# Kernel optimization log

Hardware: AMD Instinct MI355X
Metric: run time of the kernel (lower is better)

Reference implementation:

```python
import jax, jax.numpy as jnp
import numpy as np

B, L, C, H, W = 4, 16, 64, 64, 64
F, NH, NB = 128, 2, 2


def _ln(x, w, b, eps=1e-5):
    # LayerNorm over last two dims (H, W), torch-style biased variance
    m = jnp.mean(x, axis=(-2, -1), keepdims=True)
    v = jnp.var(x, axis=(-2, -1), keepdims=True)
    return (x - m) * jax.lax.rsqrt(v + eps) * w + b


def _conv2d(x, w, b):
    # x: (N, Cin, H, W), w: (Cout, Cin, k, k) -- the (1,k,k) Conv3d acts per-frame
    y = jax.lax.conv_general_dilated(x, w, (1, 1), 'SAME',
                                     dimension_numbers=('NCHW', 'OIHW', 'NCHW'))
    return y + b[None, :, None, None]


def _combine(c1, c2):
    a1, b1 = c1
    a2, b2 = c2
    return a1 * a2, a2 * b1 + b2


def _forward(x, params_log, pBw_r, pBw_i, pBb_r, pBb_i, pCw_r, pCw_i, pCb_r, pCb_i,
             lru_ln_w, lru_ln_b, cin_w, cin_b, h3_w, h3_b, h1_w, h1_b,
             h_ln_w, h_ln_b, cout_w, cout_b, ffn_ln_w, ffn_ln_b):
    gelu = lambda t: jax.nn.gelu(t, approximate=False)
    Bsz, Ln, Cc, Hh, Ww = x.shape
    for i in range(NB):
        # ---- ConvLRULayer ----
        pl = params_log[i]
        nu = jnp.exp(pl[:Cc])            # (C, H)
        theta = jnp.exp(pl[Cc:2 * Cc])   # (C, H)
        gamma = jnp.exp(pl[2 * Cc:])     # (C, H)
        lamb = jnp.exp(jax.lax.complex(-nu, theta))  # (C, H) complex
        Bw = jax.lax.complex(pBw_r[i], pBw_i[i])
        Bb = jax.lax.complex(pBb_r[i], pBb_i[i])
        Cw = jax.lax.complex(pCw_r[i], pCw_i[i])
        Cb = jax.lax.complex(pCb_r[i], pCb_i[i])
        h = jnp.fft.fft2(x.astype(jnp.complex64), axes=(-2, -1))  # (B,L,C,H,W)
        h = jnp.einsum('blchw,oc->blohw', h, Bw) + Bb[None, None, :, None, None]
        h = h * gamma[None, None, :, :, None]
        # parallel scan: h[t] = lamb * h[t-1] + h[t] along L
        a = jnp.broadcast_to(lamb[None, None, :, :, None], (Bsz, Ln, Cc, Hh, 1))
        _, h = jax.lax.associative_scan(_combine, (a, h), axis=1)
        h = jnp.fft.ifft2(h, axes=(-2, -1))
        h = jnp.einsum('blchw,oc->blohw', h, Cw) + Cb[None, None, :, None, None]
        h = _ln(h.real, lru_ln_w[i], lru_ln_b[i])
        x = h + x
        # ---- FeedForward (all Conv3d have kernel 1 in L -> per-frame 2D) ----
        y = x.reshape(Bsz * Ln, Cc, Hh, Ww)
        y_ = gelu(_conv2d(y, cin_w[i], cin_b[i]))  # (B*L, F, H, W)
        for j in range(NH):
            t = gelu(_conv2d(y_, h3_w[i, j], h3_b[i, j]))
            t = gelu(jnp.einsum('nfhw,of->nohw', t, h1_w[i, j])
                     + h1_b[i, j][None, :, None, None])
            y_ = _ln(t, h_ln_w[i, j], h_ln_b[i, j]) + y_
        t = jnp.einsum('nfhw,of->nohw', y_, cout_w[i]) + cout_b[i][None, :, None, None]
        t = _ln(t, ffn_ln_w[i], ffn_ln_b[i])
        x = t.reshape(Bsz, Ln, Cc, Hh, Ww) + x
    return x


def setup_inputs() -> dict:
    key = jax.random.key(0)
    ks = jax.random.split(key, 16)
    x = jax.random.normal(ks[0], (B, L, C, H, W), jnp.float32)
    # LRU stability init (as in the torch module)
    r_min, r_max = 0.8, 0.99
    u1 = jax.random.uniform(ks[1], (NB, C, H), jnp.float32)
    u2 = jax.random.uniform(ks[2], (NB, C, H), jnp.float32)
    nu_log = jnp.log(-0.5 * jnp.log(u1 * (r_max ** 2 - r_min ** 2) + r_min ** 2))
    theta_log = jnp.log(u2 * 2.0 * np.pi)
    gamma_log = 0.5 * jnp.log(1.0 - jnp.exp(-2.0 * jnp.exp(nu_log)))
    params_log = jnp.concatenate([nu_log, theta_log, gamma_log], axis=1)  # (NB, 3C, H)

    def nrm(k, shape, fan_in):
        return jax.random.normal(k, shape, jnp.float32) / np.sqrt(fan_in)

    return dict(
        x=x, params_log=params_log,
        pBw_r=nrm(ks[3], (NB, C, C), C), pBw_i=jnp.zeros((NB, C, C), jnp.float32),
        pBb_r=jnp.zeros((NB, C), jnp.float32), pBb_i=jnp.zeros((NB, C), jnp.float32),
        pCw_r=nrm(ks[4], (NB, C, C), C), pCw_i=jnp.zeros((NB, C, C), jnp.float32),
        pCb_r=jnp.zeros((NB, C), jnp.float32), pCb_i=jnp.zeros((NB, C), jnp.float32),
        lru_ln_w=jnp.ones((NB, H, W), jnp.float32), lru_ln_b=jnp.zeros((NB, H, W), jnp.float32),
        cin_w=nrm(ks[5], (NB, F, C, 7, 7), C * 49), cin_b=jnp.zeros((NB, F), jnp.float32),
        h3_w=nrm(ks[6], (NB, NH, F, F, 3, 3), F * 9), h3_b=jnp.zeros((NB, NH, F), jnp.float32),
        h1_w=nrm(ks[7], (NB, NH, F, F), F), h1_b=jnp.zeros((NB, NH, F), jnp.float32),
        h_ln_w=jnp.ones((NB, NH, H, W), jnp.float32), h_ln_b=jnp.zeros((NB, NH, H, W), jnp.float32),
        cout_w=nrm(ks[8], (NB, C, F), F), cout_b=jnp.zeros((NB, C), jnp.float32),
        ffn_ln_w=jnp.ones((NB, H, W), jnp.float32), ffn_ln_b=jnp.zeros((NB, H, W), jnp.float32),
    )


def reference(x, params_log, pBw_r, pBw_i, pBb_r, pBb_i, pCw_r, pCw_i, pCb_r, pCb_i,
              lru_ln_w, lru_ln_b, cin_w, cin_b, h3_w, h3_b, h1_w, h1_b,
              h_ln_w, h_ln_b, cout_w, cout_b, ffn_ln_w, ffn_ln_b):
    return _forward(x, params_log, pBw_r, pBw_i, pBb_r, pBb_i, pCw_r, pCw_i,
                    pCb_r, pCb_i, lru_ln_w, lru_ln_b, cin_w, cin_b, h3_w, h3_b,
                    h1_w, h1_b, h_ln_w, h_ln_b, cout_w, cout_b, ffn_ln_w, ffn_ln_b)
```

## Files before the change

### kernel.cpp

```cpp
#include <hip/hip_runtime.h>
#include <math.h>

static constexpr int Bd = 4, Ld = 16, Cd = 64, Hd = 64, Wd = 64, Fd = 128;
static constexpr int NBLK = 2, NHEAD = 2;
static constexpr int HW = 4096;
static constexpr float TWO_PI = 6.28318530717958647692f;

typedef __attribute__((ext_vector_type(8))) short bf16x8;
typedef __attribute__((ext_vector_type(4))) float f32x4;
typedef __attribute__((ext_vector_type(4))) unsigned int u32x4;

__device__ __forceinline__ float gelu_f(float v) {
    return 0.5f * v * (1.f + erff(v * 0.7071067811865476f));
}

__device__ __forceinline__ unsigned short bf16c(float f) {
    unsigned int u = __float_as_uint(f);
    unsigned int r = (u + 0x7fffu + ((u >> 16) & 1u)) >> 16;
    return (unsigned short)r;
}
__device__ __forceinline__ float bf2f(unsigned short u) {
    return __uint_as_float((unsigned int)u << 16);
}
__device__ __forceinline__ unsigned int packbf(float r, float i) {
// ... 73 lines not shown
        for (int q = 0; q < 4; ++q) {
            int pos = q * 64 + c;
            *(unsigned short*)(xpT + pos * 128 + ((h * 2) ^ ((c & 7) << 4))) = bf16c(vv[q]);
        }
    }
    __syncthreads();

    int w = w0 + wv;
    unsigned int* Xw = X + (size_t)fi * 262144 + (size_t)w * 4096;
    for (int half = 0; half < 2; ++half) {
        f32x4 aR[2][4], aI[2][4];
#pragma unroll
        for (int mt = 0; mt < 2; ++mt)
#pragma unroll
            for (int nt = 0; nt < 4; ++nt) { aR[mt][nt] = (f32x4)0.f; aI[mt][nt] = (f32x4)0.f; }
#pragma unroll
        for (int ks = 0; ks < 2; ++ks) {
            int koff = (ks * 64 + kg * 16);
            bf16x8 ac[2], as_[2], b[4];
#pragma unroll
            for (int mt = 0; mt < 2; ++mt) {
                int row = half * 32 + mt * 16 + pl;
                int off = row * 128 + (koff ^ ((pl & 7) << 4));
                ac[mt] = *(const bf16x8*)(tC + off);
                as_[mt] = *(const bf16x8*)(tS + off);
            }
#pragma unroll
            for (int nt = 0; nt < 4; ++nt) {
                int pos = wv * 64 + nt * 16 + pl;
                b[nt] = *(const bf16x8*)(xpT + pos * 128 + (koff ^ ((pl & 7) << 4)));
            }
#pragma unroll
            for (int mt = 0; mt < 2; ++mt)
#pragma unroll
                for (int nt = 0; nt < 4; ++nt) {
                    aR[mt][nt] = __builtin_amdgcn_mfma_f32_16x16x32_bf16(ac[mt], b[nt], aR[mt][nt], 0, 0, 0);
                    aI[mt][nt] = __builtin_amdgcn_mfma_f32_16x16x32_bf16(as_[mt], b[nt], aI[mt][nt], 0, 0, 0);
                }
        }
#pragma unroll
        for (int mt = 0; mt < 2; ++mt)
#pragma unroll
            for (int nt = 0; nt < 4; ++nt) {
                int c = nt * 16 + pl;
#pragma unroll
                for (int r = 0; r < 4; ++r) {
                    int fh = half * 32 + mt * 16 + kg * 4 + r;
                    Xw[fh * 64 + c] = packbf(aR[mt][nt][r], aI[mt][nt][r]);
                }
            }
    }
}

__global__ __launch_bounds__(256) void k_cmixm(const unsigned int* __restrict__ Xin,
                                               unsigned int* __restrict__ Xout,
                                               const unsigned short* __restrict__ wr,
                                               const unsigned short* __restrict__ wi,
                                               const float* __restrict__ gamT,
                                               const float* __restrict__ br_g,
                                               const float* __restrict__ bi_g,
                                               int use_gamma) {
    __shared__ __align__(16) unsigned char smm[65536];
    unsigned char* inr = smm;
    unsigned char* ini = smm + 16384;
    unsigned char* wR = smm + 32768;
    unsigned char* wI = smm + 40960;
    float* gam = (float*)(smm + 49152);
    int blk = blockIdx.x;
    size_t R0 = (size_t)blk * 128;
    int t = threadIdx.x, lane = t & 63, wv = t >> 6;
    int pl = lane & 15, kg = lane >> 4;
    int l3 = lane >> 3, l7 = lane & 7;

    const unsigned int* Xi = Xin + R0 * 64;
    for (int k = 0; k < 8; ++k) {
        int j = k * 256 + t;
        int row = j >> 4, c0 = (j & 15) * 4;
        u32x4 v = *(const u32x4*)(Xi + (size_t)row * 64 + c0);
        unsigned int rw0 = (v.x & 0xffffu) | (v.y << 16);
        unsigned int rw1 = (v.z & 0xffffu) | (v.w << 16);
        unsigned int iw0 = (v.x >> 16) | (v.y & 0xffff0000u);
        unsigned int iw1 = (v.z >> 16) | (v.w & 0xffff0000u);
        int off = row * 128 + ((((c0 >> 3) ^ (row & 7)) << 4) | ((c0 & 7) * 2));
        *(unsigned int*)(inr + off) = rw0;
        *(unsigned int*)(inr + off + 4) = rw1;
        *(unsigned int*)(ini + off) = iw0;
        *(unsigned int*)(ini + off + 4) = iw1;
    }
    for (int q = 0; q < 2; ++q) {
        int sg = q * 4 + wv;
        gl2lds16(wr + (size_t)(sg * 8 + l3) * 64 + (l7 ^ l3) * 8, wR + sg * 1024);
        gl2lds16(wi + (size_t)(sg * 8 + l3) * 64 + (l7 ^ l3) * 8, wI + sg * 1024);
    }
    if (use_gamma) {
        for (int j = t; j < 4096; j += 256) gam[j] = gamT[j];
    }
    __syncthreads();

    int posbase = wv * 32;
    f32x4 cR[2][4], cI[2][4];
#pragma unroll
    for (int mt = 0; mt < 2; ++mt)
#pragma unroll
        for (int nt = 0; nt < 4; ++nt) { cR[mt][nt] = (f32x4)0.f; cI[mt][nt] = (f32x4)0.f; }
#pragma unroll
    for (int ks = 0; ks < 2; ++ks) {
        int koff = ks * 64 + kg * 16;
        bf16x8 ar[2], ai[2], an[2], brf[4], bif[4];
#pragma unroll
        for (int mt = 0; mt < 2; ++mt) {
            int row = posbase + mt * 16 + pl;
            int off = row * 128 + (koff ^ ((pl & 7) << 4));
            ar[mt] = *(const bf16x8*)(inr + off);
            ai[mt] = *(const bf16x8*)(ini + off);
            an[mt] = bneg(ai[mt]);
        }
#pragma unroll
        for (int nt = 0; nt < 4; ++nt) {
            int o = nt * 16 + pl;
            int off = o * 128 + (koff ^ ((pl & 7) << 4));
            brf[nt] = *(const bf16x8*)(wR + off);
            bif[nt] = *(const bf16x8*)(wI + off);
        }
#pragma unroll
        for (int mt = 0; mt < 2; ++mt)
#pragma unroll
            for (int nt = 0; nt < 4; ++nt) {
                cR[mt][nt] = __builtin_amdgcn_mfma_f32_16x16x32_bf16(ar[mt], brf[nt], cR[mt][nt], 0, 0, 0);
                cR[mt][nt] = __builtin_amdgcn_mfma_f32_16x16x32_bf16(an[mt], bif[nt], cR[mt][nt], 0, 0, 0);
                cI[mt][nt] = __builtin_amdgcn_mfma_f32_16x16x32_bf16(ar[mt], bif[nt], cI[mt][nt], 0, 0, 0);
                cI[mt][nt] = __builtin_amdgcn_mfma_f32_16x16x32_bf16(ai[mt], brf[nt], cI[mt][nt], 0, 0, 0);
            }
    }
#pragma unroll
    for (int mt = 0; mt < 2; ++mt)
#pragma unroll
        for (int nt = 0; nt < 4; ++nt) {
            int o = nt * 16 + pl;
            float bR = 0.f, bI = 0.f;
            if (use_gamma) { bR = br_g[o]; bI = bi_g[o]; }
#pragma unroll
            for (int r = 0; r < 4; ++r) {
                int lrow = posbase + mt * 16 + kg * 4 + r;
                int prow = (blk & 31) * 128 + lrow;
                float vr = cR[mt][nt][r], vi = cI[mt][nt][r];
                if (use_gamma) {
                    if (prow < 64) { vr += bR; vi += bI; }
                    float g = gam[(prow & 63) * 64 + o];
                    vr *= g; vi *= g;
                }
                Xout[(R0 + lrow) * 64 + o] = packbf(vr, vi);
            }
        }
}

__global__ __launch_bounds__(256) void k_scan2(unsigned int* __restrict__ X,
                                               const float* __restrict__ pl) {
    int g = blockIdx.x * 256 + threadIdx.x;
    int c = g & 63;
    int fh = (g >> 6) & 63;
    int w = (g >> 12) & 63;
    int b = g >> 18;
    float nu = expf(pl[c * 64 + fh]);
    float th = expf(pl[4096 + c * 64 + fh]);
    float mag = expf(-nu);
    float sth, cth;
    sincosf(th, &sth, &cth);
    float lr = mag * cth, li = mag * sth;
    size_t base = (size_t)b * 16 * 262144 + (size_t)w * 4096 + fh * 64 + c;
    unsigned int v0 = X[base];
    float ax = bf2f((unsigned short)(v0 & 0xffffu));
    float ay = bf2f((unsigned short)(v0 >> 16));
    for (int tt = 1; tt < Ld; ++tt) {
        size_t idx = base + (size_t)tt * 262144;
        unsigned int v = X[idx];
        float vx = bf2f((unsigned short)(v & 0xffffu));
        float vy = bf2f((unsigned short)(v >> 16));
        float nr = lr * ax - li * ay + vx;
        float ni = lr * ay + li * ax + vy;
        ax = nr; ay = ni;
        X[idx] = packbf(nr, ni);
    }
}

__global__ __launch_bounds__(256) void k_idfthm_ln(const unsigned int* __restrict__ X,
                                                   const unsigned short* __restrict__ tic,
                                                   const unsigned short* __restrict__ tis,
                                                   const float* __restrict__ cbr,
                                                   const float* __restrict__ lnw,
                                                   const float* __restrict__ lnb,
                                                   const float* __restrict__ xprev,
                                                   float* __restrict__ xout) {
    __shared__ __align__(16) unsigned char smm[81920];
    unsigned char* SrT = smm;
    unsigned char* SiT = smm + 32768;
    unsigned char* tC = smm + 65536;
    unsigned char* tS = smm + 73728;
    float* y4 = (float*)smm;
    int blk = blockIdx.x;
    int fi = blk >> 4;
    int c0 = (blk & 15) * 4;
    int t = threadIdx.x, lane = t & 63, wv = t >> 6;
    int pl = lane & 15, kg = lane >> 4;
    int l3 = lane >> 3, l7 = lane & 7;

    for (int q = 0; q < 2; ++q) {
        int sg = q * 4 + wv;
        gl2lds16(tic + (size_t)(sg * 8 + l3) * 64 + (l7 ^ l3) * 8, tC + sg * 1024);
        gl2lds16(tis + (size_t)(sg * 8 + l3) * 64 + (l7 ^ l3) * 8, tS + sg * 1024);
    }
    const unsigned int* Xf = X + (size_t)fi * 262144;
    int fh = t & 63;
    for (int k = 0; k < 16; ++k) {
        int w = k * 4 + (t >> 6);
        u32x4 v = *(const u32x4*)(Xf + (size_t)w * 4096 + fh * 64 + c0);
        unsigned int vv[4] = {v.x, v.y, v.z, v.w};
#pragma unroll
        for (int cj = 0; cj < 4; ++cj) {
            int pos2 = w * 4 + cj;
            int off = pos2 * 128 + ((fh * 2) ^ ((pos2 & 7) << 4));
            *(unsigned short*)(SrT + off) = (unsigned short)(vv[cj] & 0xffffu);
            *(unsigned short*)(SiT + off) = (unsigned short)(vv[cj] >> 16);
        }
    }
    __syncthreads();

    f32x4 y[4][4];
#pragma unroll
    for (int mt = 0; mt < 4; ++mt)
#pragma unroll
        for (int nt = 0; nt < 4; ++nt) y[mt][nt] = (f32x4)0.f;
#pragma unroll
    for (int ks = 0; ks < 2; ++ks) {
        int koff = ks * 64 + kg * 16;
// ... 20 lines not shown
                y[mt][nt] = __builtin_amdgcn_mfma_f32_16x16x32_bf16(as_[mt], bif[nt], y[mt][nt], 0, 0, 0);
            }
    }
    __syncthreads();

    float cb4[4];
#pragma unroll
    for (int cj = 0; cj < 4; ++cj) cb4[cj] = cbr[c0 + cj];
#pragma unroll
    for (int mt = 0; mt < 4; ++mt)
#pragma unroll
        for (int nt = 0; nt < 4; ++nt) {
            int pos2 = wv * 64 + nt * 16 + pl;
            int w = pos2 >> 2, cj = pos2 & 3;
#pragma unroll
            for (int r = 0; r < 4; ++r) {
                int h = mt * 16 + kg * 4 + r;
                y4[cj * 4232 + h * 66 + w] = y[mt][nt][r] + cb4[cj];
            }
        }
    __syncthreads();

    int w = lane;
    const float* yp = y4 + wv * 4232;
    float s = 0.f, q = 0.f;
    for (int h = 0; h < 64; ++h) {
        float v = yp[h * 66 + w];
        s += v;
        q += v * v;
    }
#pragma unroll
    for (int off = 32; off; off >>= 1) {
        s += __shfl_xor(s, off);
        q += __shfl_xor(q, off);
    }
    float m = s * (1.f / 4096.f);
    float var = q * (1.f / 4096.f) - m * m;
    float rs = rsqrtf(var + 1e-5f);
    int c = c0 + wv;
    const float* xp = xprev + ((size_t)fi * Cd + c) * HW;
    float* xo = xout + ((size_t)fi * Cd + c) * HW;
    for (int h = 0; h < 64; ++h) {
        int p = h * 64 + w;
        xo[p] = (yp[h * 66 + w] - m) * rs * lnw[p] + lnb[p] + xp[p];
    }
}

__global__ __launch_bounds__(256) void k_ln_res(const unsigned short* __restrict__ t_in,
                                                const float* __restrict__ w,
                                                const float* __restrict__ b,
                                                float* __restrict__ dst) {
    __shared__ float red[8];
    int fr = blockIdx.x;
    const unsigned short* src = t_in + (size_t)fr * HW;
    float* d = dst + (size_t)fr * HW;
    int t = threadIdx.x;
    float vals[16];
    float s = 0.f, sq = 0.f;
#pragma unroll
    for (int j = 0; j < 16; ++j) {
        float v = bf2f(src[t + 256 * j]);
        vals[j] = v;
        s += v;
        sq += v * v;
    }
    for (int off = 32; off; off >>= 1) {
        s += __shfl_down(s, off);
        sq += __shfl_down(sq, off);
    }
    int wid = t >> 6;
    if ((t & 63) == 0) { red[wid] = s; red[4 + wid] = sq; }
    __syncthreads();
    s = red[0] + red[1] + red[2] + red[3];
    sq = red[4] + red[5] + red[6] + red[7];
    float m = s * (1.f / 4096.f);
    float var = sq * (1.f / 4096.f) - m * m;
    float rs = rsqrtf(var + 1e-5f);
#pragma unroll
    for (int j = 0; j < 16; ++j) {
        int p = t + 256 * j;
        d[p] += (vals[j] - m) * rs * w[p] + b[p];
    }
}

__global__ void k_prep7(const float* __restrict__ w, unsigned short* __restrict__ o) {
    int idx = blockIdx.x * 256 + threadIdx.x;
    if (idx < 49 * 128 * 64) {
        int tap = idx >> 13, rem = idx & 8191, f = rem >> 6, c = rem & 63;
        o[idx] = bf16c(w[(size_t)(f * 64 + c) * 49 + tap]);
    }
}
__global__ void k_prep3(const float* __restrict__ w, unsigned short* __restrict__ o,
                        int nh) {
    int idx = blockIdx.x * 256 + threadIdx.x;
    if (idx < nh * 147456) {
        int head = idx / 147456;
        int rem = idx - head * 147456;
        int tap = rem >> 14, r2 = rem & 16383, f = r2 >> 7, c = r2 & 127;
        o[idx] = bf16c(w[(size_t)head * 147456 + (size_t)(f * 128 + c) * 9 + tap]);
    }
}
__global__ void k_prepcvt(const float* __restrict__ w, unsigned short* __restrict__ o, int n) {
    int idx = blockIdx.x * 256 + threadIdx.x;
    if (idx < n) o[idx] = bf16c(w[idx]);
}

__global__ __launch_bounds__(256) void k_t2p(const float* __restrict__ x,
                                             unsigned short* __restrict__ xT) {
    __shared__ float tile[64][65];
    int blk = blockIdx.x;
    int f = blk >> 6;
    int p0 = (blk & 63) * 64;
    int t = threadIdx.x;
    const float* src = x + (size_t)f * Cd * HW;
    for (int j = t; j < 4096; j += 256) {
        int c = j >> 6, p = j & 63;
        tile[c][p] = src[(size_t)c * HW + p0 + p];
    }
    __syncthreads();
    unsigned short* dst = xT + ((size_t)f * HW + p0) * 64;
    for (int j = t; j < 4096; j += 256) {
        int p = j >> 6, c = j & 63;
        dst[(size_t)p * 64 + c] = bf16c(tile[c][p]);
    }
}

__global__ __launch_bounds__(512) void k_conv7m(const unsigned short* __restrict__ xT,
                                                const unsigned short* __restrict__ wb,
                                                const float* __restrict__ bias,
                                                unsigned short* __restrict__ yout) {
    __shared__ __align__(16) unsigned char smm[158208];
    unsigned char* inT = smm;
    unsigned char* wt0 = smm + 125440;
    int blk = blockIdx.x;
// ... 40 lines not shown
        if (tap + 1 < 49) {
            const unsigned short* g = wb + (size_t)(tap + 1) * 8192;
            unsigned char* wdst = wt0 + (cur ^ 1) * 16384;
            for (int q = 0; q < 2; ++q) {
                int sg = q * 8 + wv;
                int f = sg * 8 + l3;
                gl2lds16(g + (size_t)f * 64 + ksw_w * 8, wdst + sg * 1024);
            }
        }
        unsigned char* wcur = wt0 + cur * 16384;
        int ky = tap / 7, kx = tap % 7;
#pragma unroll
        for (int ks = 0; ks < 2; ++ks) {
            bf16x8 a[8], b[4];
#pragma unroll
            for (int m = 0; m < 8; ++m) {
                int row = wm * 2 + (m >> 2) + ky;
                int xp = (m & 3) * 16 + pl + kx;
                a[m] = *(const bf16x8*)(inT + row * 8960 + xp * 128 +
                                        (((ks * 4 + kg) ^ (xp & 7)) << 4));
            }
#pragma unroll
            for (int n = 0; n < 4; ++n) {
                int rowf = wn * 64 + n * 16 + pl;
                b[n] = *(const bf16x8*)(wcur + rowf * 128 +
                                        (((ks * 4 + kg) ^ (pl & 7)) << 4));
            }
#pragma unroll
            for (int m = 0; m < 8; ++m)
#pragma unroll
                for (int n = 0; n < 4; ++n)
                    acc[m][n] = __builtin_amdgcn_mfma_f32_16x16x32_bf16(a[m], b[n], acc[m][n], 0, 0, 0);
        }
        __syncthreads();
        cur ^= 1;
    }
    unsigned short* yo = yout + ((size_t)fi * HW + (size_t)y0 * 64) * 128;
#pragma unroll
    for (int m = 0; m < 8; ++m) {
        int rowl = wm * 2 + (m >> 2);
#pragma unroll
        for (int n = 0; n < 4; ++n) {
            int f = wn * 64 + n * 16 + pl;
            float bs = bias[f];
#pragma unroll
            for (int r = 0; r < 4; ++r) {
                int x = (m & 3) * 16 + kg * 4 + r;
                yo[(size_t)(rowl * 64 + x) * 128 + f] = bf16c(gelu_f(acc[m][n][r] + bs));
            }
        }
    }
}

__global__ __launch_bounds__(512) void k_conv3f(const unsigned short* __restrict__ yin,
                                                const unsigned short* __restrict__ wb,
                                                const float* __restrict__ bias3,
                                                const unsigned short* __restrict__ w1,
                                                const float* __restrict__ bias1,
                                                unsigned short* __restrict__ outp2,
                                                float* __restrict__ lnpart) {
    __shared__ __align__(16) unsigned char smm[134144];
    __shared__ float redS[8][64], redQ[8][64];
    unsigned char* inT = smm;
    unsigned char* wL = smm + 101376;
    int blk = blockIdx.x;
    int fi = blk >> 4;
    int y0 = (blk & 15) * 4;
    int t = threadIdx.x, lane = t & 63, wv = t >> 6;
    int l4 = lane >> 4, l15 = lane & 15;
    const unsigned short* yf = yin + (size_t)fi * HW * 128;
    float4 z4 = make_float4(0.f, 0.f, 0.f, 0.f);
    for (int seg = wv; seg < 96; seg += 8) {
        int r = seg >> 4, xs = seg & 15;
        int srow = y0 + r - 1;
        int xp = 1 + xs * 4 + l4;
        unsigned char* dst = inT + r * 16896 + (size_t)(1 + xs * 4) * 256;
        if (srow >= 0 && srow < 64) {
            int gsrc = l15 ^ (xp & 7);
            gl2lds16(yf + ((size_t)(srow * 64 + xp - 1) * 128 + gsrc * 8), dst);
        } else {
            *(float4*)(dst + lane * 16) = z4;
        }
    }
    if (t < 192) {
        int r = t / 32, k = t & 31;
        int xp = (k < 16) ? 0 : 65;
        *(float4*)(inT + r * 16896 + xp * 256 + (k & 15) * 16) = z4;
    }
    for (int sg = wv; sg < 32; sg += 8) {
        int f = sg * 4 + l4;
        gl2lds16(wb + (size_t)f * 128 + (l15 ^ (f & 7)) * 8, wL + sg * 1024);
    }
    __syncthreads();

    int wm = wv & 3, wn = wv >> 2;
    f32x4 acc[4][4];
#pragma unroll
    for (int m = 0; m < 4; ++m)
#pragma unroll
        for (int n = 0; n < 4; ++n) acc[m][n] = (f32x4)0.f;
    int kg = lane >> 4, pl = lane & 15;
    int fw = t >> 2, qw = t & 3;
    u32x4 rg[4];
    for (int tap = 0; tap < 9; ++tap) {
        if (tap < 8) {
            const u32x4* src = (const u32x4*)(wb + (size_t)(tap + 1) * 16384 +
                                              (size_t)fw * 128 + qw * 32);
#pragma unroll
            for (int j = 0; j < 4; ++j) rg[j] = src[j];
        }
        int ky = tap / 3, kx = tap % 3;
        int rbase = (wm + ky) * 16896;
#pragma unroll
        for (int ks = 0; ks < 4; ++ks) {
            bf16x8 a[4], b[4];
#pragma unroll
            for (int m = 0; m < 4; ++m) {
                int xp = m * 16 + pl + kx;
                a[m] = *(const bf16x8*)(inT + rbase + (size_t)xp * 256 +
                                        ((ks * 64 + kg * 16) ^ ((xp & 7) << 4)));
            }
#pragma unroll
            for (int n = 0; n < 4; ++n) {
                int row = wn * 64 + n * 16 + pl;
                b[n] = *(const bf16x8*)(wL + (size_t)row * 256 +
                                        ((ks * 64 + kg * 16) ^ ((pl & 7) << 4)));
            }
#pragma unroll
            for (int m = 0; m < 4; ++m)
#pragma unroll
                for (int n = 0; n < 4; ++n)
                    acc[m][n] = __builtin_amdgcn_mfma_f32_16x16x32_bf16(a[m], b[n], acc[m][n], 0, 0, 0);
        }
        __syncthreads();
        if (tap < 8) {
#pragma unroll
            for (int j = 0; j < 4; ++j)
                *(u32x4*)(wL + (size_t)fw * 256 + (((qw * 4 + j) ^ (fw & 7)) << 4)) = rg[j];
        }
        __syncthreads();
    }

    unsigned char* tL = smm;
    unsigned char* w1L = smm + 65536;
#pragma unroll
    for (int m = 0; m < 4; ++m)
#pragma unroll
        for (int n = 0; n < 4; ++n) {
            int f = wn * 64 + n * 16 + pl;
            float bs = bias3[f];
#pragma unroll
            for (int r = 0; r < 4; ++r) {
                int pos = wm * 64 + m * 16 + kg * 4 + r;
                *(unsigned short*)(tL + (size_t)pos * 256 +
                    ((((f >> 3) ^ (pos & 7)) << 4) | ((f & 7) * 2))) =
                    bf16c(gelu_f(acc[m][n][r] + bs));
            }
        }
    for (int sg = wv; sg < 32; sg += 8) {
        int rr = sg * 4 + l4;
        gl2lds16(w1 + (size_t)rr * 128 + (l15 ^ (rr & 7)) * 8, w1L + sg * 1024);
    }
    __syncthreads();

    f32x4 fa[4][4];
#pragma unroll
    for (int m = 0; m < 4; ++m)
#pragma unroll
        for (int n = 0; n < 4; ++n) fa[m][n] = (f32x4)0.f;
#pragma unroll
    for (int ks = 0; ks < 4; ++ks) {
        bf16x8 a[4], b[4];
#pragma unroll
        for (int m = 0; m < 4; ++m) {
            int row = wm * 64 + m * 16 + pl;
            a[m] = *(const bf16x8*)(tL + (size_t)row * 256 +
                                    ((ks * 64 + kg * 16) ^ ((pl & 7) << 4)));
        }
#pragma unroll
        for (int n = 0; n < 4; ++n) {
            int row = wn * 64 + n * 16 + pl;
            b[n] = *(const bf16x8*)(w1L + (size_t)row * 256 +
                                    ((ks * 64 + kg * 16) ^ ((pl & 7) << 4)));
        }
#pragma unroll
        for (int m = 0; m < 4; ++m)
#pragma unroll
            for (int n = 0; n < 4; ++n)
                fa[m][n] = __builtin_amdgcn_mfma_f32_16x16x32_bf16(a[m], b[n], fa[m][n], 0, 0, 0);
    }
    __syncthreads();

    int slab = blk & 15;
    int p0 = slab * 256;
    unsigned char* oL = smm;
#pragma unroll
    for (int n = 0; n < 4; ++n) {
        int f = wn * 64 + n * 16 + pl;
        float bs = bias1[f];
        float s = 0.f, q = 0.f;
#pragma unroll
        for (int m = 0; m < 4; ++m)
#pragma unroll
            for (int r = 0; r < 4; ++r) {
                float v = gelu_f(fa[m][n][r] + bs);
                int pos = wm * 64 + m * 16 + kg * 4 + r;
                *(unsigned short*)(oL + (size_t)pos * 256 +
                    ((((f >> 3) ^ (pos & 7)) << 4) | ((f & 7) * 2))) = bf16c(v);
                s += v;
                q += v * v;
            }
        s += __shfl_xor(s, 16); s += __shfl_xor(s, 32);
        q += __shfl_xor(q, 16); q += __shfl_xor(q, 32);
        if (kg == 0) { redS[wv][n * 16 + pl] = s; redQ[wv][n * 16 + pl] = q; }
    }
    __syncthreads();
    unsigned char* o0 = (unsigned char*)(outp2 + ((size_t)fi * HW + p0) * 128);
#pragma unroll
    for (int it = 0; it < 8; ++it) {
        int gid = it * 512 + t;
        int pos = gid >> 4, g = gid & 15;
        u32x4 v = *(const u32x4*)(oL + (size_t)pos * 256 + ((g ^ (pos & 7)) << 4));
        *(u32x4*)(o0 + (size_t)pos * 256 + g * 16) = v;
    }
    if (t < 128) {
        int wh = t >> 6, j = t & 63;
        float s = redS[wh * 4][j] + redS[wh * 4 + 1][j] + redS[wh * 4 + 2][j] + redS[wh * 4 + 3][j];
        float q = redQ[wh * 4][j] + redQ[wh * 4 + 1][j] + redQ[wh * 4 + 2][j] + redQ[wh * 4 + 3][j];
        float* lp = lnpart + ((size_t)(fi * 16 + slab) * 128 + t) * 2;
        lp[0] = s;
        lp[1] = q;
    }
}

__global__ __launch_bounds__(256) void k_lnapply2(const unsigned short* __restrict__ t2,
// ... 140 lines not shown
        for (int k = 0; k < 6; ++k) {
            size_t region = (size_t)lbs[k] * 16777216ULL;
            size_t ffn = (size_t)frs[k] * 3145728ULL;
            if (ffn > region) region = ffn;
            size_t needb = region + 1605632ULL + (size_t)frs[k] * 32768ULL + 65536ULL;
            if (needb <= ws_size) { FR = frs[k]; LB = lbs[k]; break; }
        }
    }
    size_t region = (size_t)LB * 16777216ULL;
    {
        size_t ffn = (size_t)FR * 3145728ULL;
        if (ffn > region) region = ffn;
    }
    unsigned char* ws = (unsigned char*)d_ws;
    unsigned int* Xb = (unsigned int*)ws;
    unsigned short* ybuf = (unsigned short*)ws;
    unsigned short* t2bf = (unsigned short*)(ws + (size_t)FR * 1048576);
    unsigned short* xT   = (unsigned short*)(ws + (size_t)FR * 2097152);
    unsigned short* cobuf = (unsigned short*)(ws + (size_t)FR * 2621440);
    unsigned char* wbase = ws + region;
    unsigned short* wb7  = (unsigned short*)(wbase);
    unsigned short* wb3  = (unsigned short*)(wbase + 802816);
    unsigned short* wb1  = (unsigned short*)(wbase + 1392640);
    unsigned short* wbco = (unsigned short*)(wbase + 1458176);
    unsigned short* dftT = (unsigned short*)(wbase + 1474560);
    unsigned short* lruW = (unsigned short*)(wbase + 1507328);
    float* gamT          = (float*)(wbase + 1540096);
    float* lnpart        = (float*)(wbase + 1556480);
    unsigned short* tcb = dftT;
    unsigned short* tsb = dftT + 4096;
    unsigned short* tic = dftT + 8192;
    unsigned short* tis = dftT + 12288;
    unsigned short* wBr = lruW;
    unsigned short* wBi = lruW + 4096;
    unsigned short* wCr = lruW + 8192;
    unsigned short* wCi = lruW + 12288;

    const int NCl = 4 / LB;
    const int NCf = 64 / FR;

    k_prepdft<<<64, 256, 0, stream>>>(dftT);

    for (int i = 0; i < NBLK; ++i) {
        const float* xsrc = (i == 0) ? x_in : out;

        k_preplru<<<80, 256, 0, stream>>>(pBw_r + (size_t)i * 4096,
                                          pBw_i + (size_t)i * 4096,
                                          pCw_r + (size_t)i * 4096,
                                          pCw_i + (size_t)i * 4096,
                                          pl + (size_t)i * 12288 + 8192, lruW, gamT);
        for (int cc = 0; cc < NCl; ++cc) {
            size_t boff = (size_t)cc * LB * 4194304;
            k_dfthm<<<LB * 256, 256, 0, stream>>>(xsrc + boff, Xb, tcb, tsb);
            k_cmixm<<<LB * 512, 256, 0, stream>>>(Xb, Xb, wBr, wBi, gamT,
                                                  pBb_r + (size_t)i * 64,
                                                  pBb_i + (size_t)i * 64, 1);
            k_scan2<<<LB * 1024, 256, 0, stream>>>(Xb, pl + (size_t)i * 12288);
            k_cmixm<<<LB * 512, 256, 0, stream>>>(Xb, Xb, wCr, wCi, nullptr,
                                                  nullptr, nullptr, 0);
            k_idfthm_ln<<<LB * 256, 256, 0, stream>>>(Xb, tic, tis,
                                                      pCb_r + (size_t)i * 64,
                                                      lruw + (size_t)i * 4096,
                                                      lrub + (size_t)i * 4096,
                                                      xsrc + boff, out + boff);
        }

        k_prep7<<<1568, 256, 0, stream>>>(cinw + (size_t)i * 401408, wb7);
        k_prep3<<<1152, 256, 0, stream>>>(h3w + (size_t)i * 2 * 147456, wb3, 2);
        k_prepcvt<<<128, 256, 0, stream>>>(h1w + (size_t)i * 2 * 16384, wb1, 32768);
        k_prepcvt<<<32, 256, 0, stream>>>(coutw + (size_t)i * 8192, wbco, 8192);

        for (int cc = 0; cc < NCf; ++cc) {
            float* xb = out + (size_t)cc * FR * 262144;
            k_t2p<<<FR * 64, 256, 0, stream>>>(xb, xT);
            k_conv7m<<<FR * 8, 512, 0, stream>>>(xT, wb7, cinb + (size_t)i * 128, ybuf);
            for (int j = 0; j < NHEAD; ++j) {
                k_conv3f<<<FR * 16, 512, 0, stream>>>(ybuf, wb3 + (size_t)j * 147456,
                                                      h3b + (size_t)(i * 2 + j) * 128,
                                                      wb1 + (size_t)j * 16384,
                                                      h1b + (size_t)(i * 2 + j) * 128,
                                                      t2bf, lnpart);
                k_lnapply2<<<FR * 32, 256, 0, stream>>>(t2bf, lnpart,
                                                        hlnw + (size_t)(i * 2 + j) * 4096,
                                                        hlnb + (size_t)(i * 2 + j) * 4096,
                                                        ybuf);
            }
            k_coutm<<<FR * 32, 256, 0, stream>>>(ybuf, wbco, coutb + (size_t)i * 64, cobuf);
            k_ln_res<<<FR * 64, 256, 0, stream>>>(cobuf, flnw + (size_t)i * 4096,
                                                  flnb + (size_t)i * 4096, xb);
        }
    }
}
```

Before: 1.886 ms.

## Halve conv3 LDS footprint by splitting channels into two K-passes

The fused 3x3+1x1 conv kernel now stages input and weights in two 64-channel halves instead of all 128 channels. This cuts shared memory from about 134KB to about 67KB so more blocks can be resident. The 1x1 weights are read straight from global memory instead of through LDS, and the launch bounds request more waves per unit. Separately, the LN-residual kernel moves to contiguous vectorized 16-byte loads and float4 read-modify-write. The trade-off is twice the input staging passes and barriers in the conv, plus uncached global weight reads in the 1x1 GEMM.

```diff
diff --git a/kernel.cpp b/kernel.cpp
--- a/kernel.cpp
+++ b/kernel.cpp
@@ -403,18 +403,21 @@
                                                 float* __restrict__ dst) {
     __shared__ float red[8];
     int fr = blockIdx.x;
-    const unsigned short* src = t_in + (size_t)fr * HW;
-    float* d = dst + (size_t)fr * HW;
     int t = threadIdx.x;
+    const unsigned short* src = t_in + (size_t)fr * HW + t * 16;
+    float* d = dst + (size_t)fr * HW + t * 16;
+    u32x4 v0 = *(const u32x4*)(src);
+    u32x4 v1 = *(const u32x4*)(src + 8);
     float vals[16];
+    unsigned int vw[8] = {v0.x, v0.y, v0.z, v0.w, v1.x, v1.y, v1.z, v1.w};
+#pragma unroll
+    for (int j = 0; j < 8; ++j) {
+        vals[j * 2] = bf2f((unsigned short)(vw[j] & 0xffffu));
+        vals[j * 2 + 1] = bf2f((unsigned short)(vw[j] >> 16));
+    }
     float s = 0.f, sq = 0.f;
 #pragma unroll
-    for (int j = 0; j < 16; ++j) {
-        float v = bf2f(src[t + 256 * j]);
-        vals[j] = v;
-        s += v;
-        sq += v * v;
-    }
+    for (int j = 0; j < 16; ++j) { s += vals[j]; sq += vals[j] * vals[j]; }
     for (int off = 32; off; off >>= 1) {
         s += __shfl_down(s, off);
         sq += __shfl_down(sq, off);
@@ -427,10 +430,18 @@
     float m = s * (1.f / 4096.f);
     float var = sq * (1.f / 4096.f) - m * m;
     float rs = rsqrtf(var + 1e-5f);
-#pragma unroll
-    for (int j = 0; j < 16; ++j) {
-        int p = t + 256 * j;
-        d[p] += (vals[j] - m) * rs * w[p] + b[p];
+    const float* wp = w + t * 16;
+    const float* bp = b + t * 16;
+#pragma unroll
+    for (int q4 = 0; q4 < 4; ++q4) {
+        float4 wv4 = *(const float4*)(wp + q4 * 4);
+        float4 bv4 = *(const float4*)(bp + q4 * 4);
+        float4 dv = *(const float4*)(d + q4 * 4);
+        dv.x += (vals[q4 * 4 + 0] - m) * rs * wv4.x + bv4.x;
+        dv.y += (vals[q4 * 4 + 1] - m) * rs * wv4.y + bv4.y;
+        dv.z += (vals[q4 * 4 + 2] - m) * rs * wv4.z + bv4.z;
+        dv.w += (vals[q4 * 4 + 3] - m) * rs * wv4.w + bv4.w;
+        *(float4*)(d + q4 * 4) = dv;
     }
 }
 
@@ -577,97 +588,100 @@
     }
 }
 
-__global__ __launch_bounds__(512) void k_conv3f(const unsigned short* __restrict__ yin,
-                                                const unsigned short* __restrict__ wb,
-                                                const float* __restrict__ bias3,
-                                                const unsigned short* __restrict__ w1,
-                                                const float* __restrict__ bias1,
-                                                unsigned short* __restrict__ outp2,
-                                                float* __restrict__ lnpart) {
-    __shared__ __align__(16) unsigned char smm[134144];
+__global__ __launch_bounds__(512, 4) void k_conv3f(const unsigned short* __restrict__ yin,
+                                                   const unsigned short* __restrict__ wb,
+                                                   const float* __restrict__ bias3,
+                                                   const unsigned short* __restrict__ w1,
+                                                   const float* __restrict__ bias1,
+                                                   unsigned short* __restrict__ outp2,
+                                                   float* __restrict__ lnpart) {
+    __shared__ __align__(16) unsigned char smm[67072];
     __shared__ float redS[8][64], redQ[8][64];
     unsigned char* inT = smm;
-    unsigned char* wL = smm + 101376;
+    unsigned char* wL = smm + 50688;
     int blk = blockIdx.x;
     int fi = blk >> 4;
     int y0 = (blk & 15) * 4;
     int t = threadIdx.x, lane = t & 63, wv = t >> 6;
-    int l4 = lane >> 4, l15 = lane & 15;
+    int l3 = lane >> 3, l7 = lane & 7;
+    int kg = lane >> 4, pl = lane & 15;
+    int wm = wv & 3, wn = wv >> 2;
     const unsigned short* yf = yin + (size_t)fi * HW * 128;
     float4 z4 = make_float4(0.f, 0.f, 0.f, 0.f);
-    for (int seg = wv; seg < 96; seg += 8) {
-        int r = seg >> 4, xs = seg & 15;
-        int srow = y0 + r - 1;
-        int xp = 1 + xs * 4 + l4;
-        unsigned char* dst = inT + r * 16896 + (size_t)(1 + xs * 4) * 256;
-        if (srow >= 0 && srow < 64) {
-            int gsrc = l15 ^ (xp & 7);
-            gl2lds16(yf + ((size_t)(srow * 64 + xp - 1) * 128 + gsrc * 8), dst);
-        } else {
-            *(float4*)(dst + lane * 16) = z4;
-        }
-    }
-    if (t < 192) {
-        int r = t / 32, k = t & 31;
-        int xp = (k < 16) ? 0 : 65;
-        *(float4*)(inT + r * 16896 + xp * 256 + (k & 15) * 16) = z4;
-    }
-    for (int sg = wv; sg < 32; sg += 8) {
-        int f = sg * 4 + l4;
-        gl2lds16(wb + (size_t)f * 128 + (l15 ^ (f & 7)) * 8, wL + sg * 1024);
-    }
-    __syncthreads();
-
-    int wm = wv & 3, wn = wv >> 2;
+
     f32x4 acc[4][4];
 #pragma unroll
     for (int m = 0; m < 4; ++m)
 #pragma unroll
         for (int n = 0; n < 4; ++n) acc[m][n] = (f32x4)0.f;
-    int kg = lane >> 4, pl = lane & 15;
+
     int fw = t >> 2, qw = t & 3;
-    u32x4 rg[4];
-    for (int tap = 0; tap < 9; ++tap) {
-        if (tap < 8) {
-            const u32x4* src = (const u32x4*)(wb + (size_t)(tap + 1) * 16384 +
-                                              (size_t)fw * 128 + qw * 32);
-#pragma unroll
-            for (int j = 0; j < 4; ++j) rg[j] = src[j];
-        }
-        int ky = tap / 3, kx = tap % 3;
-        int rbase = (wm + ky) * 16896;
-#pragma unroll
-        for (int ks = 0; ks < 4; ++ks) {
-            bf16x8 a[4], b[4];
-#pragma unroll
-            for (int m = 0; m < 4; ++m) {
-                int xp = m * 16 + pl + kx;
-                a[m] = *(const bf16x8*)(inT + rbase + (size_t)xp * 256 +
-                                        ((ks * 64 + kg * 16) ^ ((xp & 7) << 4)));
-            }
-#pragma unroll
-            for (int n = 0; n < 4; ++n) {
-                int row = wn * 64 + n * 16 + pl;
-                b[n] = *(const bf16x8*)(wL + (size_t)row * 256 +
-                                        ((ks * 64 + kg * 16) ^ ((pl & 7) << 4)));
-            }
-#pragma unroll
-            for (int m = 0; m < 4; ++m)
-#pragma unroll
-                for (int n = 0; n < 4; ++n)
-                    acc[m][n] = __builtin_amdgcn_mfma_f32_16x16x32_bf16(a[m], b[n], acc[m][n], 0, 0, 0);
+    for (int kp = 0; kp < 2; ++kp) {
+        for (int seg = wv; seg < 48; seg += 8) {
+            int r = seg >> 3, xg = seg & 7;
+            int srow = y0 + r - 1;
+            int xp = 1 + xg * 8 + l3;
+            unsigned char* dst = inT + r * 8448 + (size_t)(1 + xg * 8) * 128;
+            if (srow >= 0 && srow < 64) {
+                int gs = l7 ^ (xp & 7);
+                gl2lds16(yf + ((size_t)(srow * 64 + xp - 1) * 128 + kp * 64 + gs * 8), dst);
+            } else {
+                *(float4*)(dst + lane * 16) = z4;
+            }
+        }
+        if (t < 96) {
+            int r = t >> 4, k = t & 15;
+            int xp = (k < 8) ? 0 : 65;
+            *(float4*)(inT + r * 8448 + xp * 128 + (k & 7) * 16) = z4;
+        }
+        for (int sg = wv; sg < 16; sg += 8) {
+            int f = sg * 8 + l3;
+            gl2lds16(wb + (size_t)f * 128 + kp * 64 + (l7 ^ l3) * 8, wL + sg * 1024);
         }
         __syncthreads();
-        if (tap < 8) {
-#pragma unroll
-            for (int j = 0; j < 4; ++j)
-                *(u32x4*)(wL + (size_t)fw * 256 + (((qw * 4 + j) ^ (fw & 7)) << 4)) = rg[j];
-        }
-        __syncthreads();
+
+        u32x4 rg[2];
+        for (int tap = 0; tap < 9; ++tap) {
+            if (tap < 8) {
+                const unsigned short* src = wb + (size_t)(tap + 1) * 16384 +
+                                            (size_t)fw * 128 + kp * 64;
+#pragma unroll
+                for (int j = 0; j < 2; ++j) rg[j] = ((const u32x4*)src)[qw * 2 + j];
+            }
+            int ky = tap / 3, kx = tap % 3;
+            int rbase = (wm + ky) * 8448;
+#pragma unroll
+            for (int ks = 0; ks < 2; ++ks) {
+                bf16x8 a[4], b[4];
+#pragma unroll
+                for (int m = 0; m < 4; ++m) {
+                    int xp = m * 16 + pl + kx;
+                    a[m] = *(const bf16x8*)(inT + rbase + xp * 128 +
+                                            (((ks * 4 + kg) ^ (xp & 7)) << 4));
+                }
+#pragma unroll
+                for (int n = 0; n < 4; ++n) {
+                    int f = wn * 64 + n * 16 + pl;
+                    b[n] = *(const bf16x8*)(wL + f * 128 +
+                                            (((ks * 4 + kg) ^ (f & 7)) << 4));
+                }
+#pragma unroll
+                for (int m = 0; m < 4; ++m)
+#pragma unroll
+                    for (int n = 0; n < 4; ++n)
+                        acc[m][n] = __builtin_amdgcn_mfma_f32_16x16x32_bf16(a[m], b[n], acc[m][n], 0, 0, 0);
+            }
+            __syncthreads();
+            if (tap < 8) {
+#pragma unroll
+                for (int j = 0; j < 2; ++j)
+                    *(u32x4*)(wL + fw * 128 + (((qw * 2 + j) ^ (fw & 7)) << 4)) = rg[j];
+            }
+            __syncthreads();
+        }
     }
 
     unsigned char* tL = smm;
-    unsigned char* w1L = smm + 65536;
 #pragma unroll
     for (int m = 0; m < 4; ++m)
 #pragma unroll
@@ -682,10 +696,6 @@
                     bf16c(gelu_f(acc[m][n][r] + bs));
             }
         }
-    for (int sg = wv; sg < 32; sg += 8) {
-        int rr = sg * 4 + l4;
-        gl2lds16(w1 + (size_t)rr * 128 + (l15 ^ (rr & 7)) * 8, w1L + sg * 1024);
-    }
     __syncthreads();
 
     f32x4 fa[4][4];
@@ -696,16 +706,15 @@
 #pragma unroll
     for (int ks = 0; ks < 4; ++ks) {
         bf16x8 a[4], b[4];
+#pragma unroll
+        for (int n = 0; n < 4; ++n) {
+            int o = wn * 64 + n * 16 + pl;
+            b[n] = *(const bf16x8*)(w1 + (size_t)o * 128 + ks * 32 + kg * 8);
+        }
 #pragma unroll
         for (int m = 0; m < 4; ++m) {
             int row = wm * 64 + m * 16 + pl;
             a[m] = *(const bf16x8*)(tL + (size_t)row * 256 +
-                                    ((ks * 64 + kg * 16) ^ ((pl & 7) << 4)));
-        }
-#pragma unroll
-        for (int n = 0; n < 4; ++n) {
-            int row = wn * 64 + n * 16 + pl;
-            b[n] = *(const bf16x8*)(w1L + (size_t)row * 256 +
                                     ((ks * 64 + kg * 16) ^ ((pl & 7) << 4)));
         }
 #pragma unroll
```

Measured after the change: 1.932 ms. 1.02x slower.

## Fuse B-mix, temporal scan and C-mix into one LRU kernel

Applied to the files above, without the earlier changes.

Replaces the two channel-mixing MFMA kernels and the separate scan kernel with one kernel that holds a 64-row spatial slice per block. It loops over the 16 frames, keeping the scan state in registers and both weight sets in LDS, so the intermediate frames no longer round-trip through global memory three times. The cost is a grid of only LB*64 blocks with a serial 16-step loop, extra syncthreads and more LDS per block, which lowers parallelism and occupancy. A separate change vectorizes the LayerNorm residual kernel to contiguous 16-element per-thread loads and stores.

```diff
diff --git a/kernel.cpp b/kernel.cpp
--- a/kernel.cpp
+++ b/kernel.cpp
@@ -149,134 +149,163 @@
     }
 }
 
-__global__ __launch_bounds__(256) void k_cmixm(const unsigned int* __restrict__ Xin,
-                                               unsigned int* __restrict__ Xout,
-                                               const unsigned short* __restrict__ wr,
-                                               const unsigned short* __restrict__ wi,
-                                               const float* __restrict__ gamT,
-                                               const float* __restrict__ br_g,
-                                               const float* __restrict__ bi_g,
-                                               int use_gamma) {
-    __shared__ __align__(16) unsigned char smm[65536];
+__global__ __launch_bounds__(256) void k_lrumid(unsigned int* __restrict__ X,
+                                                const unsigned short* __restrict__ wbr,
+                                                const unsigned short* __restrict__ wbi,
+                                                const unsigned short* __restrict__ wcr,
+                                                const unsigned short* __restrict__ wci,
+                                                const float* __restrict__ gamT,
+                                                const float* __restrict__ br_g,
+                                                const float* __restrict__ bi_g,
+                                                const float* __restrict__ plg) {
+    __shared__ __align__(16) unsigned char smm[81920];
     unsigned char* inr = smm;
-    unsigned char* ini = smm + 16384;
-    unsigned char* wR = smm + 32768;
-    unsigned char* wI = smm + 40960;
-    float* gam = (float*)(smm + 49152);
+    unsigned char* ini = smm + 8192;
+    unsigned char* hre = smm + 16384;
+    unsigned char* him = smm + 24576;
+    unsigned char* wBR = smm + 32768;
+    unsigned char* wBI = smm + 40960;
+    unsigned char* wCR = smm + 49152;
+    unsigned char* wCI = smm + 57344;
+    float* gam = (float*)(smm + 65536);
     int blk = blockIdx.x;
-    size_t R0 = (size_t)blk * 128;
+    int b = blk >> 6, s = blk & 63;
     int t = threadIdx.x, lane = t & 63, wv = t >> 6;
-    int pl = lane & 15, kg = lane >> 4;
+    int pj = lane & 15, kg = lane >> 4;
     int l3 = lane >> 3, l7 = lane & 7;
 
-    const unsigned int* Xi = Xin + R0 * 64;
-    for (int k = 0; k < 8; ++k) {
-        int j = k * 256 + t;
-        int row = j >> 4, c0 = (j & 15) * 4;
-        u32x4 v = *(const u32x4*)(Xi + (size_t)row * 64 + c0);
-        unsigned int rw0 = (v.x & 0xffffu) | (v.y << 16);
-        unsigned int rw1 = (v.z & 0xffffu) | (v.w << 16);
-        unsigned int iw0 = (v.x >> 16) | (v.y & 0xffff0000u);
-        unsigned int iw1 = (v.z >> 16) | (v.w & 0xffff0000u);
-        int off = row * 128 + ((((c0 >> 3) ^ (row & 7)) << 4) | ((c0 & 7) * 2));
-        *(unsigned int*)(inr + off) = rw0;
-        *(unsigned int*)(inr + off + 4) = rw1;
-        *(unsigned int*)(ini + off) = iw0;
-        *(unsigned int*)(ini + off + 4) = iw1;
-    }
     for (int q = 0; q < 2; ++q) {
         int sg = q * 4 + wv;
-        gl2lds16(wr + (size_t)(sg * 8 + l3) * 64 + (l7 ^ l3) * 8, wR + sg * 1024);
-        gl2lds16(wi + (size_t)(sg * 8 + l3) * 64 + (l7 ^ l3) * 8, wI + sg * 1024);
-    }
-    if (use_gamma) {
-        for (int j = t; j < 4096; j += 256) gam[j] = gamT[j];
-    }
-    __syncthreads();
-
-    int posbase = wv * 32;
-    f32x4 cR[2][4], cI[2][4];
-#pragma unroll
-    for (int mt = 0; mt < 2; ++mt)
-#pragma unroll
-        for (int nt = 0; nt < 4; ++nt) { cR[mt][nt] = (f32x4)0.f; cI[mt][nt] = (f32x4)0.f; }
-#pragma unroll
-    for (int ks = 0; ks < 2; ++ks) {
-        int koff = ks * 64 + kg * 16;
-        bf16x8 ar[2], ai[2], an[2], brf[4], bif[4];
-#pragma unroll
-        for (int mt = 0; mt < 2; ++mt) {
-            int row = posbase + mt * 16 + pl;
-            int off = row * 128 + (koff ^ ((pl & 7) << 4));
-            ar[mt] = *(const bf16x8*)(inr + off);
-            ai[mt] = *(const bf16x8*)(ini + off);
-            an[mt] = bneg(ai[mt]);
+        size_t goff = (size_t)(sg * 8 + l3) * 64 + (l7 ^ l3) * 8;
+        gl2lds16(wbr + goff, wBR + sg * 1024);
+        gl2lds16(wbi + goff, wBI + sg * 1024);
+        gl2lds16(wcr + goff, wCR + sg * 1024);
+        gl2lds16(wci + goff, wCI + sg * 1024);
+    }
+    for (int j = t; j < 4096; j += 256) gam[j] = gamT[j];
+
+    float lamr[4][4], lami[4][4];
+#pragma unroll
+    for (int nt = 0; nt < 4; ++nt) {
+        int o = nt * 16 + pj;
+#pragma unroll
+        for (int r = 0; r < 4; ++r) {
+            int fh = wv * 16 + kg * 4 + r;
+            float nu = expf(plg[o * 64 + fh]);
+            float th = expf(plg[4096 + o * 64 + fh]);
+            float mag = expf(-nu);
+            float sth, cth;
+            sincosf(th, &sth, &cth);
+            lamr[nt][r] = mag * cth;
+            lami[nt][r] = mag * sth;
+        }
+    }
+    float bRo[4], bIo[4];
+#pragma unroll
+    for (int nt = 0; nt < 4; ++nt) {
+        bRo[nt] = (s == 0) ? br_g[nt * 16 + pj] : 0.f;
+        bIo[nt] = (s == 0) ? bi_g[nt * 16 + pj] : 0.f;
+    }
+    float str[4][4], sti[4][4];
+    unsigned int* Xfrm = X + (size_t)b * 16 * 262144 + (size_t)s * 4096;
+
+    for (int l = 0; l < 16; ++l) {
+        unsigned int* Xi = Xfrm + (size_t)l * 262144;
+        __syncthreads();
+        for (int k = 0; k < 4; ++k) {
+            int j = k * 256 + t;
+            int row = j >> 4, c0 = (j & 15) * 4;
+            u32x4 v = *(const u32x4*)(Xi + (size_t)row * 64 + c0);
+            unsigned int rw0 = (v.x & 0xffffu) | (v.y << 16);
+            unsigned int rw1 = (v.z & 0xffffu) | (v.w << 16);
+            unsigned int iw0 = (v.x >> 16) | (v.y & 0xffff0000u);
+            unsigned int iw1 = (v.z >> 16) | (v.w & 0xffff0000u);
+            int off = row * 128 + ((((c0 >> 3) ^ (row & 7)) << 4) | ((c0 & 7) * 2));
+            *(unsigned int*)(inr + off) = rw0;
+            *(unsigned int*)(inr + off + 4) = rw1;
+            *(unsigned int*)(ini + off) = iw0;
+            *(unsigned int*)(ini + off + 4) = iw1;
+        }
+        __syncthreads();
+
+        f32x4 cR[4], cI[4];
+#pragma unroll
+        for (int nt = 0; nt < 4; ++nt) { cR[nt] = (f32x4)0.f; cI[nt] = (f32x4)0.f; }
+#pragma unroll
+        for (int ks = 0; ks < 2; ++ks) {
+            int koff = ks * 64 + kg * 16;
+            int aoff = (wv * 16 + pj) * 128 + (koff ^ ((pj & 7) << 4));
+            bf16x8 ar = *(const bf16x8*)(inr + aoff);
+            bf16x8 ai = *(const bf16x8*)(ini + aoff);
+            bf16x8 an = bneg(ai);
+#pragma unroll
+            for (int nt = 0; nt < 4; ++nt) {
+                int o = nt * 16 + pj;
+                int woff = o * 128 + (koff ^ ((pj & 7) << 4));
+                bf16x8 brf = *(const bf16x8*)(wBR + woff);
+                bf16x8 bif = *(const bf16x8*)(wBI + woff);
+                cR[nt] = __builtin_amdgcn_mfma_f32_16x16x32_bf16(ar, brf, cR[nt], 0, 0, 0);
+                cR[nt] = __builtin_amdgcn_mfma_f32_16x16x32_bf16(an, bif, cR[nt], 0, 0, 0);
+                cI[nt] = __builtin_amdgcn_mfma_f32_16x16x32_bf16(ar, bif, cI[nt], 0, 0, 0);
+                cI[nt] = __builtin_amdgcn_mfma_f32_16x16x32_bf16(ai, brf, cI[nt], 0, 0, 0);
+            }
         }
 #pragma unroll
         for (int nt = 0; nt < 4; ++nt) {
-            int o = nt * 16 + pl;
-            int off = o * 128 + (koff ^ ((pl & 7) << 4));
-            brf[nt] = *(const bf16x8*)(wR + off);
-            bif[nt] = *(const bf16x8*)(wI + off);
-        }
-#pragma unroll
-        for (int mt = 0; mt < 2; ++mt)
+            int o = nt * 16 + pj;
+#pragma unroll
+            for (int r = 0; r < 4; ++r) {
+                int row = wv * 16 + kg * 4 + r;
+                float g = gam[row * 64 + o];
+                float vr = (cR[nt][r] + bRo[nt]) * g;
+                float vi = (cI[nt][r] + bIo[nt]) * g;
+                if (l == 0) {
+                    str[nt][r] = vr;
+                    sti[nt][r] = vi;
+                } else {
+                    float nr = lamr[nt][r] * str[nt][r] - lami[nt][r] * sti[nt][r] + vr;
+                    float ni = lamr[nt][r] * sti[nt][r] + lami[nt][r] * str[nt][r] + vi;
+                    str[nt][r] = nr;
+                    sti[nt][r] = ni;
+                }
+                int hoff = row * 128 + ((((o >> 3) ^ (row & 7)) << 4) | ((o & 7) * 2));
+                *(unsigned short*)(hre + hoff) = bf16c(str[nt][r]);
+                *(unsigned short*)(him + hoff) = bf16c(sti[nt][r]);
+            }
+        }
+        __syncthreads();
+
+        f32x4 dR[4], dI[4];
+#pragma unroll
+        for (int nt = 0; nt < 4; ++nt) { dR[nt] = (f32x4)0.f; dI[nt] = (f32x4)0.f; }
+#pragma unroll
+        for (int ks = 0; ks < 2; ++ks) {
+            int koff = ks * 64 + kg * 16;
+            int aoff = (wv * 16 + pj) * 128 + (koff ^ ((pj & 7) << 4));
+            bf16x8 ar = *(const bf16x8*)(hre + aoff);
+            bf16x8 ai = *(const bf16x8*)(him + aoff);
+            bf16x8 an = bneg(ai);
 #pragma unroll
             for (int nt = 0; nt < 4; ++nt) {
-                cR[mt][nt] = __builtin_amdgcn_mfma_f32_16x16x32_bf16(ar[mt], brf[nt], cR[mt][nt], 0, 0, 0);
-                cR[mt][nt] = __builtin_amdgcn_mfma_f32_16x16x32_bf16(an[mt], bif[nt], cR[mt][nt], 0, 0, 0);
-                cI[mt][nt] = __builtin_amdgcn_mfma_f32_16x16x32_bf16(ar[mt], bif[nt], cI[mt][nt], 0, 0, 0);
-                cI[mt][nt] = __builtin_amdgcn_mfma_f32_16x16x32_bf16(ai[mt], brf[nt], cI[mt][nt], 0, 0, 0);
-            }
-    }
-#pragma unroll
-    for (int mt = 0; mt < 2; ++mt)
+                int o = nt * 16 + pj;
+                int woff = o * 128 + (koff ^ ((pj & 7) << 4));
+                bf16x8 brf = *(const bf16x8*)(wCR + woff);
+                bf16x8 bif = *(const bf16x8*)(wCI + woff);
+                dR[nt] = __builtin_amdgcn_mfma_f32_16x16x32_bf16(ar, brf, dR[nt], 0, 0, 0);
+                dR[nt] = __builtin_amdgcn_mfma_f32_16x16x32_bf16(an, bif, dR[nt], 0, 0, 0);
+                dI[nt] = __builtin_amdgcn_mfma_f32_16x16x32_bf16(ar, bif, dI[nt], 0, 0, 0);
+                dI[nt] = __builtin_amdgcn_mfma_f32_16x16x32_bf16(ai, brf, dI[nt], 0, 0, 0);
+            }
+        }
 #pragma unroll
         for (int nt = 0; nt < 4; ++nt) {
-            int o = nt * 16 + pl;
-            float bR = 0.f, bI = 0.f;
-            if (use_gamma) { bR = br_g[o]; bI = bi_g[o]; }
+            int o = nt * 16 + pj;
 #pragma unroll
             for (int r = 0; r < 4; ++r) {
-                int lrow = posbase + mt * 16 + kg * 4 + r;
-                int prow = (blk & 31) * 128 + lrow;
-                float vr = cR[mt][nt][r], vi = cI[mt][nt][r];
-                if (use_gamma) {
-                    if (prow < 64) { vr += bR; vi += bI; }
-                    float g = gam[(prow & 63) * 64 + o];
-                    vr *= g; vi *= g;
-                }
-                Xout[(R0 + lrow) * 64 + o] = packbf(vr, vi);
-            }
-        }
-}
-
-__global__ __launch_bounds__(256) void k_scan2(unsigned int* __restrict__ X,
-                                               const float* __restrict__ pl) {
-    int g = blockIdx.x * 256 + threadIdx.x;
-    int c = g & 63;
-    int fh = (g >> 6) & 63;
-    int w = (g >> 12) & 63;
-    int b = g >> 18;
-    float nu = expf(pl[c * 64 + fh]);
-    float th = expf(pl[4096 + c * 64 + fh]);
-    float mag = expf(-nu);
-    float sth, cth;
-    sincosf(th, &sth, &cth);
-    float lr = mag * cth, li = mag * sth;
-    size_t base = (size_t)b * 16 * 262144 + (size_t)w * 4096 + fh * 64 + c;
-    unsigned int v0 = X[base];
-    float ax = bf2f((unsigned short)(v0 & 0xffffu));
-    float ay = bf2f((unsigned short)(v0 >> 16));
-    for (int tt = 1; tt < Ld; ++tt) {
-        size_t idx = base + (size_t)tt * 262144;
-        unsigned int v = X[idx];
-        float vx = bf2f((unsigned short)(v & 0xffffu));
-        float vy = bf2f((unsigned short)(v >> 16));
-        float nr = lr * ax - li * ay + vx;
-        float ni = lr * ay + li * ax + vy;
-        ax = nr; ay = ni;
-        X[idx] = packbf(nr, ni);
+                int row = wv * 16 + kg * 4 + r;
+                Xi[(size_t)row * 64 + o] = packbf(dR[nt][r], dI[nt][r]);
+            }
+        }
     }
 }
 
@@ -403,18 +432,21 @@
                                                 float* __restrict__ dst) {
     __shared__ float red[8];
     int fr = blockIdx.x;
-    const unsigned short* src = t_in + (size_t)fr * HW;
-    float* d = dst + (size_t)fr * HW;
     int t = threadIdx.x;
+    const unsigned short* src = t_in + (size_t)fr * HW + t * 16;
+    float* d = dst + (size_t)fr * HW + t * 16;
+    u32x4 v0 = *(const u32x4*)(src);
+    u32x4 v1 = *(const u32x4*)(src + 8);
     float vals[16];
+    unsigned int vw[8] = {v0.x, v0.y, v0.z, v0.w, v1.x, v1.y, v1.z, v1.w};
+#pragma unroll
+    for (int j = 0; j < 8; ++j) {
+        vals[j * 2] = bf2f((unsigned short)(vw[j] & 0xffffu));
+        vals[j * 2 + 1] = bf2f((unsigned short)(vw[j] >> 16));
+    }
     float s = 0.f, sq = 0.f;
 #pragma unroll
-    for (int j = 0; j < 16; ++j) {
-        float v = bf2f(src[t + 256 * j]);
-        vals[j] = v;
-        s += v;
-        sq += v * v;
-    }
+    for (int j = 0; j < 16; ++j) { s += vals[j]; sq += vals[j] * vals[j]; }
     for (int off = 32; off; off >>= 1) {
         s += __shfl_down(s, off);
         sq += __shfl_down(sq, off);
@@ -427,10 +459,18 @@
     float m = s * (1.f / 4096.f);
     float var = sq * (1.f / 4096.f) - m * m;
     float rs = rsqrtf(var + 1e-5f);
-#pragma unroll
-    for (int j = 0; j < 16; ++j) {
-        int p = t + 256 * j;
-        d[p] += (vals[j] - m) * rs * w[p] + b[p];
+    const float* wp = w + t * 16;
+    const float* bp = b + t * 16;
+#pragma unroll
+    for (int q4 = 0; q4 < 4; ++q4) {
+        float4 wv4 = *(const float4*)(wp + q4 * 4);
+        float4 bv4 = *(const float4*)(bp + q4 * 4);
+        float4 dv = *(const float4*)(d + q4 * 4);
+        dv.x += (vals[q4 * 4 + 0] - m) * rs * wv4.x + bv4.x;
+        dv.y += (vals[q4 * 4 + 1] - m) * rs * wv4.y + bv4.y;
+        dv.z += (vals[q4 * 4 + 2] - m) * rs * wv4.z + bv4.z;
+        dv.w += (vals[q4 * 4 + 3] - m) * rs * wv4.w + bv4.w;
+        *(float4*)(d + q4 * 4) = dv;
     }
 }
 
@@ -952,12 +992,10 @@
         for (int cc = 0; cc < NCl; ++cc) {
             size_t boff = (size_t)cc * LB * 4194304;
             k_dfthm<<<LB * 256, 256, 0, stream>>>(xsrc + boff, Xb, tcb, tsb);
-            k_cmixm<<<LB * 512, 256, 0, stream>>>(Xb, Xb, wBr, wBi, gamT,
+            k_lrumid<<<LB * 64, 256, 0, stream>>>(Xb, wBr, wBi, wCr, wCi, gamT,
                                                   pBb_r + (size_t)i * 64,
-                                                  pBb_i + (size_t)i * 64, 1);
-            k_scan2<<<LB * 1024, 256, 0, stream>>>(Xb, pl + (size_t)i * 12288);
-            k_cmixm<<<LB * 512, 256, 0, stream>>>(Xb, Xb, wCr, wCi, nullptr,
-                                                  nullptr, nullptr, 0);
+                                                  pBb_i + (size_t)i * 64,
+                                                  pl + (size_t)i * 12288);
             k_idfthm_ln<<<LB * 256, 256, 0, stream>>>(Xb, tic, tis,
                                                       pCb_r + (size_t)i * 64,
                                                       lruw + (size_t)i * 4096,
```

New measurement: 1.856 ms. About the same (-1.6%).
